# Performance work log

Measured on AMD Instinct MI355X. Metric: run time of the kernel, lower is better.

The kernel has to match this reference:

```python
import jax, jax.numpy as jnp
import numpy as np

N_NODES = 100000
D_FEAT = 128
N_EDGES = 1600000


def setup_inputs() -> dict:
    key = jax.random.key(0)
    k1, k2, k3 = jax.random.split(key, 3)
    x = jax.random.normal(k1, (N_NODES, D_FEAT), dtype=jnp.float32)
    edge_weight = jax.random.uniform(k2, (N_EDGES,), dtype=jnp.float32)
    edge_index = jax.random.randint(k3, (2, N_EDGES), 0, N_NODES, dtype=jnp.int64)
    return {"x": x, "edge_weight": edge_weight, "edge_index": edge_index, "n_nodes": N_NODES}


def reference(x, edge_weight, edge_index, n_nodes):
    # h_v = sum_{(u->v) in E} w_uv * h_u  (gather -> scale -> scatter_add)
    src = edge_index[0]
    dst = edge_index[1]
    msg = x[src] * edge_weight[:, None]          # (E, d)
    out = jax.ops.segment_sum(msg, dst, num_segments=n_nodes)  # (N, d)
    return out
```

## Files before the change

kernel.cpp:

```cpp
#include <hip/hip_runtime.h>
#include <math.h>


constexpr int D_FEAT = 128;
constexpr int NPB = 64;
constexpr int LOG_NPB = 6;
constexpr int NBK_MAX = 2048;
constexpr int HBLK = 256;
constexpr int SCB = 256;
constexpr int CAP = 1536;

typedef float v4f __attribute__((ext_vector_type(4)));

__global__ __launch_bounds__(256) void scatter_atomic_kernel(
    const float* __restrict__ x, const float* __restrict__ w,
    const int* __restrict__ src_idx, const int* __restrict__ dst_idx,
    float* __restrict__ out, int n_edges) {
  long long tid = (long long)blockIdx.x * blockDim.x + threadIdx.x;
  int lane = (int)(tid & 31);
  long long e = tid >> 5;
  if (e >= n_edges) return;
  int s = src_idx[e];
  int d = dst_idx[e];
  float wt = w[e];
  float4 v = ((const float4*)(x + (size_t)s * D_FEAT))[lane];
  float* o = out + (size_t)d * D_FEAT + (size_t)lane * 4;
  atomicAdd(o + 0, v.x * wt);
  atomicAdd(o + 1, v.y * wt);
  atomicAdd(o + 2, v.z * wt);
  atomicAdd(o + 3, v.w * wt);
}

__device__ __forceinline__ int block_excl_scan(int v, int* sh, int* total) {
  const int lane = threadIdx.x & 63;
  const int wid = threadIdx.x >> 6;
  const int nw = blockDim.x >> 6;
  int inc = v;
  #pragma unroll
  for (int o = 1; o < 64; o <<= 1) {
    int t = __shfl_up(inc, o, 64);
    if (lane >= o) inc += t;
  }
  if (lane == 63) sh[wid] = inc;
  __syncthreads();
  if (threadIdx.x == 0) {
    int a = 0;
    for (int k = 0; k < nw; ++k) { int t = sh[k]; sh[k] = a; a += t; }
    sh[nw] = a;
  }
  __syncthreads();
  int r = sh[wid] + inc - v;
  if (total) *total = sh[nw];
  __syncthreads();
  return r;
}

__global__ __launch_bounds__(512) void hist_kernel(
    const int* __restrict__ dst, int* __restrict__ gtot,
    int* __restrict__ gcur, int* __restrict__ gbase, int* __restrict__ done,
    int n_edges, int nbk, int tile) {
  __shared__ int h[NBK_MAX];
  __shared__ int sh[9];
  __shared__ int slast;
  const int tid = threadIdx.x;
  const int b = blockIdx.x;
  for (int k = tid; k < nbk; k += 512) h[k] = 0;
  __syncthreads();
  int base = b * tile;
  int lim = min(base + tile, n_edges);
  for (int i = base + tid; i < lim; i += 512)
    atomicAdd(&h[((unsigned)dst[i]) >> LOG_NPB], 1);
  __syncthreads();
  for (int k = tid; k < nbk; k += 512)
    if (h[k]) atomicAdd(&gtot[k], h[k]);
  __threadfence();
  __syncthreads();
  if (tid == 0)
    slast = (__hip_atomic_fetch_add(done, 1, __ATOMIC_ACQ_REL,
                                    __HIP_MEMORY_SCOPE_AGENT) ==
             (int)gridDim.x - 1);
  __syncthreads();
  if (slast) {
    int carry = 0;
    for (int kb = 0; kb < nbk; kb += 512) {
      int k = kb + tid;
      int v = (k < nbk)
                  ? __hip_atomic_load(&gtot[k], __ATOMIC_RELAXED,
                                      __HIP_MEMORY_SCOPE_AGENT)
                  : 0;
      int tot;
      int ex = block_excl_scan(v, sh, &tot);
      if (k < nbk) { gbase[k] = carry + ex; gcur[k] = carry + ex; }
      carry += tot;
    }
    if (tid == 0) gbase[nbk] = carry;
  }
}

__global__ __launch_bounds__(256) void init_seg_kernel(int* __restrict__ gcur,
                                                       int nbk, int capb) {
  int k = blockIdx.x * 256 + threadIdx.x;
  if (k < nbk) gcur[k] = k * capb;
}

__global__ __launch_bounds__(512) void scatter_kernel(
    const int* __restrict__ src, const int* __restrict__ dst,
    const float* __restrict__ w, int* __restrict__ gcur,
    uint2* __restrict__ csr, int n_edges, int nbk, int tile, int capb) {
  __shared__ int h[NBK_MAX];
  __shared__ int cur[NBK_MAX];
  __shared__ int gb[NBK_MAX];
  const int tid = threadIdx.x;
  const int b = blockIdx.x;
  int base = b * tile;
  int lim = min(base + tile, n_edges);
  for (int k = tid; k < nbk; k += 512) h[k] = 0;
  __syncthreads();
  for (int i = base + tid; i < lim; i += 512)
    atomicAdd(&h[((unsigned)dst[i]) >> LOG_NPB], 1);
  __syncthreads();
  for (int k = tid; k < nbk; k += 512) {
    cur[k] = 0;
    int v = h[k];
    if (v) gb[k] = atomicAdd(&gcur[k], v);
  }
  __syncthreads();
  for (int i = base + tid; i < lim; i += 512) {
    unsigned d = (unsigned)dst[i];
    unsigned k = d >> LOG_NPB;
    int pos = gb[k] + atomicAdd(&cur[k], 1);
    if (capb == 0 || pos < (int)(k + 1) * capb)
      csr[pos] = make_uint2((unsigned)src[i] | ((d & (NPB - 1u)) << 20),
                            __float_as_uint(w[i]));
  }
}

__global__ __launch_bounds__(256) void gather_kernel(
    const float* __restrict__ x, const int* __restrict__ gbase,
    const int* __restrict__ gcur, const uint2* __restrict__ csr,
    float* __restrict__ out, int n_nodes, int capb,
    const int* __restrict__ src, const int* __restrict__ dst,
    const float* __restrict__ w, int n_edges) {
  __shared__ uint2 eds[CAP];
  __shared__ unsigned short perm[CAP];
  __shared__ int loff[NPB + 1];
  __shared__ int lcur[NPB];
  __shared__ int sh[9];

  const int b = blockIdx.x;
  const int tid = threadIdx.x;
  const int beg = capb ? b * capb : gbase[b];
  const int cnt = gcur[b] - beg;
  const int limcap = capb ? capb : CAP;
  const int nbase = b * NPB;

  const int wv = tid >> 6;
  const int lane = tid & 63;
  const int f = lane & 31;
  const int half = lane >> 5;
  const float4* X = (const float4*)x;

  if (cnt <= limcap) {
    if (tid < NPB) lcur[tid] = 0;
    __syncthreads();
    for (int i = tid; i < cnt; i += 256) {
      uint2 e = csr[beg + i];
      eds[i] = e;
      atomicAdd(&lcur[e.x >> 20], 1);
    }
    __syncthreads();
    {
      int v = (tid < NPB) ? lcur[tid] : 0;
      int ex = block_excl_scan(v, sh, nullptr);
      __syncthreads();
      if (tid < NPB) { loff[tid] = ex; lcur[tid] = 0; }
      if (tid == 0) loff[NPB] = cnt;
    }
    __syncthreads();
    for (int i = tid; i < cnt; i += 256) {
      int dl = eds[i].x >> 20;
      int pos = loff[dl] + atomicAdd(&lcur[dl], 1);
      perm[pos] = (unsigned short)i;
    }
    __syncthreads();

    for (int n = wv; n < NPB; n += 4) {
      int node = nbase + n;
      if (node >= n_nodes) break;
      int jb = loff[n];
      int je = loff[n + 1];
      float4 a0 = make_float4(0.f, 0.f, 0.f, 0.f);
      float4 a1 = make_float4(0.f, 0.f, 0.f, 0.f);
      float4 a2 = make_float4(0.f, 0.f, 0.f, 0.f);
      float4 a3 = make_float4(0.f, 0.f, 0.f, 0.f);
      int j = jb + half;
      for (; j + 6 < je; j += 8) {
        uint2 e0 = eds[perm[j]];
        uint2 e1 = eds[perm[j + 2]];
        uint2 e2 = eds[perm[j + 4]];
        uint2 e3 = eds[perm[j + 6]];
        float4 v0 = X[(size_t)(e0.x & 0xFFFFFu) * 32 + f];
        float4 v1 = X[(size_t)(e1.x & 0xFFFFFu) * 32 + f];
        float4 v2 = X[(size_t)(e2.x & 0xFFFFFu) * 32 + f];
        float4 v3 = X[(size_t)(e3.x & 0xFFFFFu) * 32 + f];
        float w0 = __uint_as_float(e0.y);
        float w1 = __uint_as_float(e1.y);
        float w2 = __uint_as_float(e2.y);
        float w3 = __uint_as_float(e3.y);
        a0.x += w0 * v0.x; a0.y += w0 * v0.y; a0.z += w0 * v0.z; a0.w += w0 * v0.w;
        a1.x += w1 * v1.x; a1.y += w1 * v1.y; a1.z += w1 * v1.z; a1.w += w1 * v1.w;
        a2.x += w2 * v2.x; a2.y += w2 * v2.y; a2.z += w2 * v2.z; a2.w += w2 * v2.w;
        a3.x += w3 * v3.x; a3.y += w3 * v3.y; a3.z += w3 * v3.z; a3.w += w3 * v3.w;
      }
      for (; j < je; j += 2) {
        uint2 e0 = eds[perm[j]];
        float4 v0 = X[(size_t)(e0.x & 0xFFFFFu) * 32 + f];
        float w0 = __uint_as_float(e0.y);
        a0.x += w0 * v0.x; a0.y += w0 * v0.y; a0.z += w0 * v0.z; a0.w += w0 * v0.w;
      }
      a0.x += a1.x + a2.x + a3.x;
      a0.y += a1.y + a2.y + a3.y;
      a0.z += a1.z + a2.z + a3.z;
      a0.w += a1.w + a2.w + a3.w;
      a0.x += __shfl_xor(a0.x, 32, 64);
      a0.y += __shfl_xor(a0.y, 32, 64);
      a0.z += __shfl_xor(a0.z, 32, 64);
      a0.w += __shfl_xor(a0.w, 32, 64);
      if (half == 0) {
        v4f val = {a0.x, a0.y, a0.z, a0.w};
        __builtin_nontemporal_store(val, (v4f*)out + (size_t)node * 32 + f);
      }
    }
  } else {
    for (int n = wv; n < NPB; n += 4) {
      int node = nbase + n;
      if (node >= n_nodes) break;
      float4 a0 = make_float4(0.f, 0.f, 0.f, 0.f);
      for (int j = half; j < n_edges; j += 2) {
        if (dst[j] == node) {
          float4 v = X[(size_t)src[j] * 32 + f];
          float wt = w[j];
          a0.x += wt * v.x; a0.y += wt * v.y; a0.z += wt * v.z; a0.w += wt * v.w;
        }
      }
      a0.x += __shfl_xor(a0.x, 32, 64);
      a0.y += __shfl_xor(a0.y, 32, 64);
      a0.z += __shfl_xor(a0.z, 32, 64);
      a0.w += __shfl_xor(a0.w, 32, 64);
      if (half == 0) {
        v4f val = {a0.x, a0.y, a0.z, a0.w};
        __builtin_nontemporal_store(val, (v4f*)out + (size_t)node * 32 + f);
      }
    }
  }
}

extern "C" void kernel_launch(void* const* d_in, const int* in_sizes, int n_in,
                              void* d_out, int out_size, void* d_ws, size_t ws_size,
                              hipStream_t stream) {
  const float* x  = (const float*)d_in[0];
  const float* w  = (const float*)d_in[1];
  const int* eidx = (const int*)d_in[2];

  int n_edges = in_sizes[1];
  int n_nodes = out_size / D_FEAT;
  const int* src = eidx;
  const int* dst = eidx + n_edges;
  float* out = (float*)d_out;

  if (n_edges <= 0) {
    hipMemsetAsync(d_out, 0, (size_t)out_size * sizeof(float), stream);
    return;
  }

  const int nbk = (n_nodes + NPB - 1) / NPB;
  const int stile = (n_edges + SCB - 1) / SCB;
  const int htile = (n_edges + HBLK - 1) / HBLK;

  const size_t ctrl_ints = (size_t)NBK_MAX + NBK_MAX + 4 + (NBK_MAX + 4);
  const size_t ctrl_bytes = ctrl_ints * 4;
  long long slots_avail =
      ((long long)ws_size - (long long)ctrl_bytes) / 8;

  long long mean = n_edges / (nbk > 0 ? nbk : 1);
  int capb_min = (int)(mean + 7.0 * sqrt((double)(mean > 0 ? mean : 1)) + 32);
  int capb = 0;
  if (nbk > 0 && slots_avail > 0) {
    long long c = slots_avail / nbk;
    if (c > CAP) c = CAP;
    capb = (int)(c & ~7LL);
  }
  bool seg_ok = (capb >= capb_min);
  bool exact_ok = (slots_avail >= (long long)n_edges);

  if ((!seg_ok && !exact_ok) || nbk > NBK_MAX || n_nodes >= (1 << 20)) {
    hipMemsetAsync(d_out, 0, (size_t)out_size * sizeof(float), stream);
    long long total_threads = (long long)n_edges * 32;
    long long grid = (total_threads + 255) / 256;
    scatter_atomic_kernel<<<(dim3)(unsigned)grid, 256, 0, stream>>>(
        x, w, src, dst, out, n_edges);
    return;
  }

  int* gtot = (int*)d_ws;
  int* gcur = gtot + NBK_MAX;
  int* done = gcur + NBK_MAX;
  int* gbase = done + 4;
  uint2* csr = (uint2*)(gbase + NBK_MAX + 4);

  if (seg_ok) {
    init_seg_kernel<<<(nbk + 255) / 256, 256, 0, stream>>>(gcur, nbk, capb);
    scatter_kernel<<<SCB, 512, 0, stream>>>(src, dst, w, gcur, csr,
                                            n_edges, nbk, stile, capb);
    gather_kernel<<<nbk, 256, 0, stream>>>(x, gbase, gcur, csr, out, n_nodes,
                                           capb, src, dst, w, n_edges);
  } else {
    hipMemsetAsync(gtot, 0, (size_t)(NBK_MAX * 2 + 4) * sizeof(int), stream);
    hist_kernel<<<HBLK, 512, 0, stream>>>(dst, gtot, gcur, gbase, done,
                                          n_edges, nbk, htile);
    scatter_kernel<<<SCB, 512, 0, stream>>>(src, dst, w, gcur, csr,
                                            n_edges, nbk, stile, 0);
    gather_kernel<<<nbk, 256, 0, stream>>>(x, gbase, gcur, csr, out, n_nodes,
                                           0, src, dst, w, n_edges);
  }
}
```

Measured before the change: 254.3 us.

## Widen node buckets and pad per-block CSR runs to 8-edge alignment

Buckets grow from 64 to 128 nodes (fewer, larger segments with a larger shared-memory edge cap) and the scatter grid drops from 256 to 128 blocks. Each block's run within a bucket is rounded up to a multiple of 8 entries and filled with zero-weight dummy edges, so writes and later reads of CSR runs stay aligned. The capacity check is now done once per block-bucket instead of per edge. This adds padding slots and extra dummy edges for the gather to process, and fewer scatter blocks may reduce parallelism.

```diff
diff --git a/kernel.cpp b/kernel.cpp
--- a/kernel.cpp
+++ b/kernel.cpp
@@ -3,12 +3,11 @@
 
 
 constexpr int D_FEAT = 128;
-constexpr int NPB = 64;
-constexpr int LOG_NPB = 6;
-constexpr int NBK_MAX = 2048;
-constexpr int HBLK = 256;
-constexpr int SCB = 256;
-constexpr int CAP = 1536;
+constexpr int NPB = 128;
+constexpr int LOG_NPB = 7;
+constexpr int NBK_MAX = 1024;
+constexpr int SCB = 128;
+constexpr int CAP = 3072;
 
 typedef float v4f __attribute__((ext_vector_type(4)));
 
@@ -58,7 +57,7 @@
 __global__ __launch_bounds__(512) void hist_kernel(
     const int* __restrict__ dst, int* __restrict__ gtot,
     int* __restrict__ gcur, int* __restrict__ gbase, int* __restrict__ done,
-    int n_edges, int nbk, int tile) {
+    int n_edges, int nbk, int tile, int pad8) {
   __shared__ int h[NBK_MAX];
   __shared__ int sh[9];
   __shared__ int slast;
@@ -71,8 +70,13 @@
   for (int i = base + tid; i < lim; i += 512)
     atomicAdd(&h[((unsigned)dst[i]) >> LOG_NPB], 1);
   __syncthreads();
-  for (int k = tid; k < nbk; k += 512)
-    if (h[k]) atomicAdd(&gtot[k], h[k]);
+  for (int k = tid; k < nbk; k += 512) {
+    int v = h[k];
+    if (v) {
+      int r = pad8 ? ((v + 7) & ~7) : v;
+      atomicAdd(&gtot[k], r);
+    }
+  }
   __threadfence();
   __syncthreads();
   if (tid == 0)
@@ -106,7 +110,8 @@
 __global__ __launch_bounds__(512) void scatter_kernel(
     const int* __restrict__ src, const int* __restrict__ dst,
     const float* __restrict__ w, int* __restrict__ gcur,
-    uint2* __restrict__ csr, int n_edges, int nbk, int tile, int capb) {
+    uint2* __restrict__ csr, int n_edges, int nbk, int tile, int capb,
+    int pad8) {
   __shared__ int h[NBK_MAX];
   __shared__ int cur[NBK_MAX];
   __shared__ int gb[NBK_MAX];
@@ -122,16 +127,29 @@
   for (int k = tid; k < nbk; k += 512) {
     cur[k] = 0;
     int v = h[k];
-    if (v) gb[k] = atomicAdd(&gcur[k], v);
+    if (v) {
+      int r = pad8 ? ((v + 7) & ~7) : v;
+      int g = atomicAdd(&gcur[k], r);
+      if (capb && (g + r > (k + 1) * capb)) g = -1;
+      gb[k] = g;
+      if (g >= 0) {
+        for (int p = v; p < r; ++p)
+          csr[g + p] =
+              make_uint2(((unsigned)(g + p) & (NPB - 1u)) << 20, 0u);
+      }
+    } else {
+      gb[k] = -1;
+    }
   }
   __syncthreads();
   for (int i = base + tid; i < lim; i += 512) {
     unsigned d = (unsigned)dst[i];
     unsigned k = d >> LOG_NPB;
-    int pos = gb[k] + atomicAdd(&cur[k], 1);
-    if (capb == 0 || pos < (int)(k + 1) * capb)
-      csr[pos] = make_uint2((unsigned)src[i] | ((d & (NPB - 1u)) << 20),
-                            __float_as_uint(w[i]));
+    int pos = atomicAdd(&cur[k], 1);
+    int g = gb[k];
+    if (g >= 0)
+      csr[g + pos] = make_uint2((unsigned)src[i] | ((d & (NPB - 1u)) << 20),
+                                __float_as_uint(w[i]));
   }
 }
 
@@ -275,22 +293,23 @@
 
   const int nbk = (n_nodes + NPB - 1) / NPB;
   const int stile = (n_edges + SCB - 1) / SCB;
-  const int htile = (n_edges + HBLK - 1) / HBLK;
 
   const size_t ctrl_ints = (size_t)NBK_MAX + NBK_MAX + 4 + (NBK_MAX + 4);
   const size_t ctrl_bytes = ctrl_ints * 4;
-  long long slots_avail =
-      ((long long)ws_size - (long long)ctrl_bytes) / 8;
+  long long slots_avail = ((long long)ws_size - (long long)ctrl_bytes) / 8;
 
   long long mean = n_edges / (nbk > 0 ? nbk : 1);
-  int capb_min = (int)(mean + 7.0 * sqrt((double)(mean > 0 ? mean : 1)) + 32);
+  int capb_min = (int)(mean + 7.0 * sqrt((double)(mean > 0 ? mean : 1)) +
+                       3.5 * SCB + 8.0 * sqrt((double)SCB) + 16);
   int capb = 0;
   if (nbk > 0 && slots_avail > 0) {
     long long c = slots_avail / nbk;
     if (c > CAP) c = CAP;
     capb = (int)(c & ~7LL);
   }
-  bool seg_ok = (capb >= capb_min);
+  long long worst_pad = (long long)SCB * nbk * 7;
+  bool seg_ok = (capb >= capb_min && capb_min <= CAP);
+  bool exact_pad_ok = (slots_avail >= (long long)n_edges + worst_pad + 16);
   bool exact_ok = (slots_avail >= (long long)n_edges);
 
   if ((!seg_ok && !exact_ok) || nbk > NBK_MAX || n_nodes >= (1 << 20)) {
@@ -311,15 +330,16 @@
   if (seg_ok) {
     init_seg_kernel<<<(nbk + 255) / 256, 256, 0, stream>>>(gcur, nbk, capb);
     scatter_kernel<<<SCB, 512, 0, stream>>>(src, dst, w, gcur, csr,
-                                            n_edges, nbk, stile, capb);
+                                            n_edges, nbk, stile, capb, 1);
     gather_kernel<<<nbk, 256, 0, stream>>>(x, gbase, gcur, csr, out, n_nodes,
                                            capb, src, dst, w, n_edges);
   } else {
+    int pad8 = exact_pad_ok ? 1 : 0;
     hipMemsetAsync(gtot, 0, (size_t)(NBK_MAX * 2 + 4) * sizeof(int), stream);
-    hist_kernel<<<HBLK, 512, 0, stream>>>(dst, gtot, gcur, gbase, done,
-                                          n_edges, nbk, htile);
+    hist_kernel<<<SCB, 512, 0, stream>>>(dst, gtot, gcur, gbase, done,
+                                         n_edges, nbk, stile, pad8);
     scatter_kernel<<<SCB, 512, 0, stream>>>(src, dst, w, gcur, csr,
-                                            n_edges, nbk, stile, 0);
+                                            n_edges, nbk, stile, 0, pad8);
     gather_kernel<<<nbk, 256, 0, stream>>>(x, gbase, gcur, csr, out, n_nodes,
                                            0, src, dst, w, n_edges);
   }
```

Measured after the change: 262.8 us. 1.03x slower.
